# Performance work log

Hardware: AMD Instinct MI355X
Metric: run time of the kernel (lower is better)

## Reference

```python
import jax, jax.numpy as jnp
import numpy as np

N = 50000
E = 800000
EPS = 1e-5
# per-layer (in_dim, heads, out_dim, concat) matching GraphEncoder defaults
LAYERS = [(16, 4, 32, True), (128, 4, 32, True), (128, 4, 32, True), (128, 1, 128, False)]


def setup_inputs() -> dict:
    key = jax.random.key(0)
    ks = jax.random.split(key, 32)
    rn = lambda k, shape: jax.random.normal(k, shape, jnp.float32) * 0.1
    inp = {}
    inp["node_types"] = jax.random.randint(ks[0], (N,), 0, 3)
    inp["edge_index"] = jax.random.randint(ks[1], (2, E), 0, N)
    inp["emb"] = rn(ks[2], (3, 16))
    i = 3
    for li, (ind, h, od, _) in enumerate(LAYERS):
        inp[f"Wl{li}"] = rn(ks[i], (ind, h * od)); i += 1
        inp[f"Wr{li}"] = rn(ks[i], (ind, h * od)); i += 1
        inp[f"att{li}"] = rn(ks[i], (h, od)); i += 1
        inp[f"b{li}"] = rn(ks[i], (h * od if li < 3 else od,)); i += 1
    inp["ln_g"] = jnp.ones((4, 128), jnp.float32)
    inp["ln_b"] = jnp.zeros((4, 128), jnp.float32)
    return inp


def gatv2_layer(x, src, dst, Wl, Wr, att, b, heads, out_dim, concat):
    # PyG GATv2Conv (share_weights=False, negative_slope=0.2, self-loops added by caller)
    n = x.shape[0]
    xl = (x @ Wl).reshape(n, heads, out_dim)  # source transform (messages)
    xr = (x @ Wr).reshape(n, heads, out_dim)  # target transform
    e = jax.nn.leaky_relu(xl[src] + xr[dst], 0.2)          # [E', H, D]
    logit = jnp.einsum('ehd,hd->eh', e, att)               # [E', H]
    lmax = jax.ops.segment_max(logit, dst, num_segments=n)  # segment softmax over dst
    p = jnp.exp(logit - lmax[dst])
    z = jax.ops.segment_sum(p, dst, num_segments=n)
    alpha = p / z[dst]                                      # every node has a self-loop -> z > 0
    out = jax.ops.segment_sum(xl[src] * alpha[..., None], dst, num_segments=n)  # [n, H, D]
    out = out.reshape(n, heads * out_dim) if concat else out.mean(axis=1)
    return out + b


def layer_norm(x, g, b):
    mu = x.mean(-1, keepdims=True)
    var = ((x - mu) ** 2).mean(-1, keepdims=True)
    return (x - mu) / jnp.sqrt(var + EPS) * g + b


def reference(node_types, edge_index, emb, Wl0, Wr0, att0, b0, Wl1, Wr1, att1, b1,
              Wl2, Wr2, att2, b2, Wl3, Wr3, att3, b3, ln_g, ln_b):
    n = node_types.shape[0]
    loops = jnp.arange(n)
    src = jnp.concatenate([edge_index[0], loops])
    dst = jnp.concatenate([edge_index[1], loops])
    x = emb[node_types]
    params = [(Wl0, Wr0, att0, b0), (Wl1, Wr1, att1, b1), (Wl2, Wr2, att2, b2), (Wl3, Wr3, att3, b3)]
    for li, ((Wl, Wr, att, b), (_, h, od, concat)) in enumerate(zip(params, LAYERS)):
        res = x
        x = gatv2_layer(x, src, dst, Wl, Wr, att, b, h, od, concat)
        if x.shape[-1] == res.shape[-1]:
            x = x + res
        x = jax.nn.relu(layer_norm(x, ln_g[li], ln_b[li]))
    return x
```

## Files before the change

### kernel.cpp

```cpp
#include <hip/hip_runtime.h>

__global__ void GraphEncoder_20555713479231_kernel() {}

using hfrag8 = __attribute__((ext_vector_type(8))) _Float16;
using facc4  = __attribute__((ext_vector_type(4))) float;
using h2     = __attribute__((ext_vector_type(2))) _Float16;

__device__ __forceinline__ unsigned short f2h_bits(float f) {
  union { _Float16 h; unsigned short u; } c;
  c.h = (_Float16)f;
  return c.u;
}
__device__ __forceinline__ unsigned packh(float a, float b) {
  return (unsigned)f2h_bits(a) | ((unsigned)f2h_bits(b) << 16);
}
__device__ __forceinline__ h2 u2h(unsigned u) {
  union { unsigned u; h2 h; } c;
  c.u = u;
  return c.h;
}
__device__ __forceinline__ unsigned h22u(h2 h) {
  union { h2 h; unsigned u; } c;
  c.h = h;
  return c.u;
}
__device__ __forceinline__ float h2f_lo(unsigned u) { return (float)u2h(u).x; }
__device__ __forceinline__ float h2f_hi(unsigned u) { return (float)u2h(u).y; }

__global__ __launch_bounds__(256) void k_hist(const int* __restrict__ dst,
                                              int* __restrict__ deg, int e) {
  int i = blockIdx.x * blockDim.x + threadIdx.x;
  if (i < e) atomicAdd(&deg[dst[i]], 1);
}

__global__ __launch_bounds__(256) void k_scan1(const int* __restrict__ deg,
                                               int* __restrict__ off,
                                               int* __restrict__ bsum, int n) {
  __shared__ int wsum[4];
  int tid = threadIdx.x;
  int gid = blockIdx.x * 256 + tid;
  int lane = tid & 63, wid = tid >> 6;
  int v = (gid < n) ? (deg[gid] + 1) : 0;
  int x = v;
  #pragma unroll
  for (int d = 1; d < 64; d <<= 1) {
    int t = __shfl_up(x, d);
    if (lane >= d) x += t;
  }
  if (lane == 63) wsum[wid] = x;
  __syncthreads();
  int wpre = 0;
  for (int k = 0; k < wid; ++k) wpre += wsum[k];
  if (gid < n) off[gid] = wpre + x - v;
  if (tid == 0) {
    int t = 0;
    #pragma unroll
    for (int k = 0; k < 4; ++k) t += wsum[k];
    bsum[blockIdx.x] = t;
  }
}

__global__ __launch_bounds__(256) void k_scan2(int* __restrict__ bsum,
                                               int* __restrict__ off, int nb, int n) {
  __shared__ int wsum[4];
  int tid = threadIdx.x;
  int lane = tid & 63, wid = tid >> 6;
  int v = (tid < nb) ? bsum[tid] : 0;
  int x = v;
  #pragma unroll
  for (int d = 1; d < 64; d <<= 1) {
    int t = __shfl_up(x, d);
    if (lane >= d) x += t;
  }
  if (lane == 63) wsum[wid] = x;
  __syncthreads();
  int wpre = 0;
  for (int k = 0; k < wid; ++k) wpre += wsum[k];
  if (tid < nb) bsum[tid] = wpre + x - v;
  if (tid == 0) {
    int t = 0;
    #pragma unroll
    for (int k = 0; k < 4; ++k) t += wsum[k];
    off[n] = t;
  }
}

__global__ __launch_bounds__(256) void k_scan3(int* __restrict__ off,
                                               const int* __restrict__ bsum,
                                               int* __restrict__ pos,
                                               int* __restrict__ csr, int n) {
  int gid = blockIdx.x * 256 + threadIdx.x;
  if (gid < n) {
    int o = off[gid] + bsum[blockIdx.x];
    off[gid] = o;
    csr[o] = gid;
    pos[gid] = o + 1;
  }
}

__global__ __launch_bounds__(256) void k_fill(const int* __restrict__ src,
                                              const int* __restrict__ dst,
                                              int* __restrict__ pos,
                                              int* __restrict__ csr, int e) {
  int i = blockIdx.x * blockDim.x + threadIdx.x;
  if (i < e) {
    int d = dst[i];
    int p = atomicAdd(&pos[d], 1);
    csr[p] = src[i];
  }
}

__global__ __launch_bounds__(256)
void k_pack3(const float* __restrict__ wl1, const float* __restrict__ wr1,
             const float* __restrict__ wl2, const float* __restrict__ wr2,
             const float* __restrict__ wl3, const float* __restrict__ wr3,
             const float* __restrict__ emb,
             const float* __restrict__ wl0, const float* __restrict__ wr0,
             unsigned short* __restrict__ bp,
             unsigned* __restrict__ tlb, float* __restrict__ trf) {
  int b = blockIdx.x;
  if (b < 384) {
    int idx = b * 256 + threadIdx.x;
    int layer = idx >> 15;
    int r = idx & 32767;
    int j = r & 7, lane = (r >> 3) & 63, ct = (r >> 9) & 15, t = r >> 13;
    int k = t * 32 + (lane >> 4) * 8 + j;
    int c = ct * 16 + (lane & 15);
    const float* wl = (layer == 0) ? wl1 : ((layer == 1) ? wl2 : wl3);
    const float* wr = (layer == 0) ? wr1 : ((layer == 1) ? wr2 : wr3);
    float v = (c < 128) ? wl[k * 128 + c] : wr[k * 128 + (c - 128)];
    bp[idx] = f2h_bits(v);
  } else {
    int tid = threadIdx.x;
    if (tid >= 192) return;
    int row = tid >> 6, cp = tid & 63, c0 = cp * 2;
    float al0 = 0.f, al1 = 0.f, ar0 = 0.f, ar1 = 0.f;
    #pragma unroll
    for (int k = 0; k < 16; ++k) {
      float ev = emb[row * 16 + k];
      al0 += ev * wl0[k * 128 + c0];
      al1 += ev * wl0[k * 128 + c0 + 1];
      ar0 += ev * wr0[k * 128 + c0];
      ar1 += ev * wr0[k * 128 + c0 + 1];
    }
    tlb[row * 64 + cp] = packh(al0, al1);
    *(float2*)(trf + row * 128 + c0) = make_float2(ar0, ar1);
  }
}

__global__ __launch_bounds__(256)
void k_agg0(const int* __restrict__ off, const int* __restrict__ csr,
            const int* __restrict__ types,
            const unsigned* __restrict__ tlb, const float* __restrict__ trf,
            const float* __restrict__ att, const float* __restrict__ bias,
            const float* __restrict__ lng, const float* __restrict__ lnb,
            unsigned* __restrict__ yout, int n) {
  int v = (blockIdx.x * blockDim.x + threadIdx.x) >> 6;
  int lane = threadIdx.x & 63;
  if (v >= n) return;
  v = __builtin_amdgcn_readfirstlane(v);
  int beg = off[v], end = off[v + 1];
  int c0 = 0, c1 = 0, c2 = 0;
  for (int base = beg; base < end; base += 64) {
    int e = base + lane;
    bool act = e < end;
    int u = act ? csr[e] : 0;
    int ty = act ? types[u] : 3;
    c0 += __popcll(__ballot(ty == 0));
    c1 += __popcll(__ballot(ty == 1));
    c2 += __popcll(__ballot(ty == 2));
  }
  float cnt[3] = {(float)c0, (float)c1, (float)c2};
  int f0 = lane * 2;
  int tyv = types[v];
  float2 xrv = *(const float2*)(trf + tyv * 128 + f0);
  float a0 = att[f0], a1 = att[f0 + 1];
  float s = 0.f, O0 = 0.f, O1 = 0.f;
  #pragma unroll
  for (int ty = 0; ty < 3; ++ty) {
    unsigned p = tlb[ty * 64 + lane];
    float x0 = h2f_lo(p), x1 = h2f_hi(p);
    float t0 = x0 + xrv.x; t0 = t0 > 0.f ? t0 : 0.2f * t0;
    float t1 = x1 + xrv.y; t1 = t1 > 0.f ? t1 : 0.2f * t1;
    float c = t0 * a0 + t1 * a1;
    c += __shfl_xor(c, 1);
    c += __shfl_xor(c, 2);
    c += __shfl_xor(c, 4);
    c += __shfl_xor(c, 8);
    float w = cnt[ty] * __expf(c);
    s += w;
    O0 = fmaf(w, x0, O0);
    O1 = fmaf(w, x1, O1);
  }
  float inv = 1.f / s;
  float o0 = O0 * inv + bias[f0];
  float o1 = O1 * inv + bias[f0 + 1];
  float sum = o0 + o1, sq = o0 * o0 + o1 * o1;
  #pragma unroll
  for (int d2 = 1; d2 < 64; d2 <<= 1) {
    sum += __shfl_xor(sum, d2);
    sq += __shfl_xor(sq, d2);
  }
  float mu = sum * (1.f / 128.f);
  float var = sq * (1.f / 128.f) - mu * mu;
  float rstd = rsqrtf(var + 1e-5f);
  float y0 = fmaxf((o0 - mu) * rstd * lng[f0] + lnb[f0], 0.f);
  float y1 = fmaxf((o1 - mu) * rstd * lng[f0 + 1] + lnb[f0 + 1], 0.f);
  yout[(size_t)v * 64 + lane] = packh(y0, y1);
}

__global__ __launch_bounds__(256)
void k_gemm(const unsigned* __restrict__ x, const unsigned short* __restrict__ bp,
            unsigned* __restrict__ xlo, unsigned* __restrict__ xro, int nstrips, int n) {
  int wave = (blockIdx.x * 256 + threadIdx.x) >> 6;
  int lane = threadIdx.x & 63;
  if (wave >= nstrips) return;
  int r0 = wave * 16;
  int row = r0 + (lane & 15);
  if (row >= n) row = n - 1;
  int quad = lane >> 4;
  const unsigned* ap = x + (size_t)row * 64;
  hfrag8 a[4];
  #pragma unroll
  for (int t = 0; t < 4; ++t) a[t] = *(const hfrag8*)(ap + t * 16 + quad * 4);
  unsigned short* xloS = (unsigned short*)xlo;
  unsigned short* xroS = (unsigned short*)xro;
  int rbase = r0 + quad * 4;
  #pragma unroll
  for (int ct = 0; ct < 16; ++ct) {
    facc4 acc = {0.f, 0.f, 0.f, 0.f};
    #pragma unroll
    for (int t = 0; t < 4; ++t) {
      hfrag8 b = *(const hfrag8*)(bp + (size_t)(((t * 16 + ct) * 64 + lane) * 8));
      acc = __builtin_amdgcn_mfma_f32_16x16x32_f16(a[t], b, acc, 0, 0, 0);
    }
    int col = (ct & 7) * 16 + (lane & 15);
    unsigned short* dstp = (ct < 8) ? xloS : xroS;
    #pragma unroll
    for (int i = 0; i < 4; ++i) {
      int r = rbase + i;
      if (r < n) dstp[(size_t)r * 128 + col] = f2h_bits(acc[i]);
    }
  }
}

__global__ __launch_bounds__(256)
void k_agg(const int* __restrict__ off, const int* __restrict__ csr,
           const unsigned* __restrict__ xl, const unsigned* __restrict__ xr,
           const float* __restrict__ att, const float* __restrict__ bias,
           const unsigned* __restrict__ xres,
           const float* __restrict__ lng, const float* __restrict__ lnb,
           unsigned* __restrict__ ybf, float* __restrict__ yf32, int n, int wide) {
  int v = (blockIdx.x * blockDim.x + threadIdx.x) >> 6;
  int lane = threadIdx.x & 63;
  if (v >= n) return;
  v = __builtin_amdgcn_readfirstlane(v);
  int f0 = lane * 2;
  h2 a2;
  a2.x = (_Float16)att[f0];
  a2.y = (_Float16)att[f0 + 1];
  h2 r2 = u2h(xr[(size_t)v * 64 + lane]);
  h2 k02 = {(_Float16)0.2f, (_Float16)0.2f};
  int beg = off[v], end = off[v + 1];
  int last = end - 1;
  const unsigned* xlp = xl + lane;
  int iA = csr[beg];
  int iB = csr[min(beg + 1, last)];
  int iC = csr[min(beg + 2, last)];
  int iD = csr[min(beg + 3, last)];
  unsigned pA = xlp[(size_t)iA * 64];
  unsigned pB = xlp[(size_t)iB * 64];
  unsigned pC = xlp[(size_t)iC * 64];
  unsigned pD = xlp[(size_t)iD * 64];
  float sa = 0.f, Oa0 = 0.f, Oa1 = 0.f;
  float sb = 0.f, Ob0 = 0.f, Ob1 = 0.f;
  for (int e = beg; e < end; e += 2) {
    int i4 = csr[min(e + 4, last)];
    int i5 = csr[min(e + 5, last)];
    unsigned p4 = xlp[(size_t)i4 * 64];
    unsigned p5 = xlp[(size_t)i5 * 64];
    h2 xa = u2h(pA), xb = u2h(pB);
    h2 ta = xa + r2;
    h2 tb = xb + r2;
    h2 la = __builtin_elementwise_max(ta, ta * k02);
    h2 lb = __builtin_elementwise_max(tb, tb * k02);
    h2 da = la * a2;
    h2 db = lb * a2;
    h2 cp;
    cp.x = da.x + da.y;
    cp.y = db.x + db.y;
    unsigned cu = h22u(cp);
    cu = h22u(u2h(cu) + u2h((unsigned)__shfl_xor((int)cu, 1)));
    cu = h22u(u2h(cu) + u2h((unsigned)__shfl_xor((int)cu, 2)));
    cu = h22u(u2h(cu) + u2h((unsigned)__shfl_xor((int)cu, 4)));
    cu = h22u(u2h(cu) + u2h((unsigned)__shfl_xor((int)cu, 8)));
    if (wide) {
      cu = h22u(u2h(cu) + u2h((unsigned)__shfl_xor((int)cu, 16)));
      cu = h22u(u2h(cu) + u2h((unsigned)__shfl_xor((int)cu, 32)));
    }
    h2 cf = u2h(cu);
    float wa = __expf((float)cf.x);
    float wb = (e + 1 < end) ? __expf((float)cf.y) : 0.f;
    sa += wa; Oa0 = fmaf(wa, (float)xa.x, Oa0); Oa1 = fmaf(wa, (float)xa.y, Oa1);
    sb += wb; Ob0 = fmaf(wb, (float)xb.x, Ob0); Ob1 = fmaf(wb, (float)xb.y, Ob1);
    pA = pC; pB = pD; pC = p4; pD = p5;
  }
  float s = sa + sb;
  float O0 = Oa0 + Ob0, O1 = Oa1 + Ob1;
  float inv = 1.f / s;
  float o0 = O0 * inv + bias[f0];
  float o1 = O1 * inv + bias[f0 + 1];
  if (xres) {
    unsigned rs = xres[(size_t)v * 64 + lane];
    o0 += h2f_lo(rs);
    o1 += h2f_hi(rs);
  }
  float sum = o0 + o1, sq = o0 * o0 + o1 * o1;
  #pragma unroll
  for (int d2 = 1; d2 < 64; d2 <<= 1) {
    sum += __shfl_xor(sum, d2);
    sq += __shfl_xor(sq, d2);
  }
  float mu = sum * (1.f / 128.f);
  float var = sq * (1.f / 128.f) - mu * mu;
  float rstd = rsqrtf(var + 1e-5f);
  float y0 = fmaxf((o0 - mu) * rstd * lng[f0] + lnb[f0], 0.f);
  float y1 = fmaxf((o1 - mu) * rstd * lng[f0 + 1] + lnb[f0 + 1], 0.f);
  if (yf32) {
    *(float2*)(yf32 + (size_t)v * 128 + f0) = make_float2(y0, y1);
  } else {
    ybf[(size_t)v * 64 + lane] = packh(y0, y1);
  }
}

extern "C" void kernel_launch(void* const* d_in, const int* in_sizes, int n_in,
                              void* d_out, int out_size, void* d_ws, size_t ws_size,
                              hipStream_t stream) {
  (void)n_in; (void)out_size; (void)ws_size;
  const int* node_types = (const int*)d_in[0];
  const int* edge_index = (const int*)d_in[1];
  const float* emb = (const float*)d_in[2];
  const float* Wl0 = (const float*)d_in[3];
  const float* Wr0 = (const float*)d_in[4];
  const float* att0 = (const float*)d_in[5];
  const float* b0 = (const float*)d_in[6];
  const float* Wl1 = (const float*)d_in[7];
  const float* Wr1 = (const float*)d_in[8];
  const float* att1 = (const float*)d_in[9];
  const float* b1 = (const float*)d_in[10];
  const float* Wl2 = (const float*)d_in[11];
  const float* Wr2 = (const float*)d_in[12];
  const float* att2 = (const float*)d_in[13];
  const float* b2 = (const float*)d_in[14];
  const float* Wl3 = (const float*)d_in[15];
  const float* Wr3 = (const float*)d_in[16];
  const float* att3 = (const float*)d_in[17];
  const float* b3 = (const float*)d_in[18];
  const float* lng = (const float*)d_in[19];
  const float* lnb = (const float*)d_in[20];

  int n = in_sizes[0];
  int e = in_sizes[1] / 2;
  const int* srcp = edge_index;
  const int* dstp = edge_index + e;
  int nblocks = (n + 255) / 256;

  char* wsp = (char*)d_ws;
  size_t ofs = 0;
  int* deg = (int*)(wsp + ofs); ofs += (((size_t)n * 4) + 255) & ~(size_t)255;
  int* off = (int*)(wsp + ofs); ofs += (((size_t)(n + 1) * 4) + 255) & ~(size_t)255;
  int* csr = (int*)(wsp + ofs); ofs += (((size_t)(e + n) * 4) + 255) & ~(size_t)255;
  int* bsum = (int*)(wsp + ofs); ofs += (((size_t)nblocks * 4) + 255) & ~(size_t)255;
  unsigned* xlb = (unsigned*)(wsp + ofs); ofs += (((size_t)n * 64 * 4) + 255) & ~(size_t)255;
  unsigned* xrb = (unsigned*)(wsp + ofs); ofs += (((size_t)n * 64 * 4) + 255) & ~(size_t)255;
  unsigned* xcur = (unsigned*)(wsp + ofs); ofs += (((size_t)n * 64 * 4) + 255) & ~(size_t)255;
  unsigned short* bp = (unsigned short*)(wsp + ofs); ofs += 3 * 65536;
  unsigned* tlb = (unsigned*)(wsp + ofs); ofs += 1024;
  float* trf = (float*)(wsp + ofs); ofs += 2048;
  int* pos = deg;

  (void)hipMemsetAsync(deg, 0, (size_t)n * 4, stream);
  k_hist<<<(e + 255) / 256, 256, 0, stream>>>(dstp, deg, e);
  k_pack3<<<385, 256, 0, stream>>>(Wl1, Wr1, Wl2, Wr2, Wl3, Wr3,
                                   emb, Wl0, Wr0, bp, tlb, trf);
  k_scan1<<<nblocks, 256, 0, stream>>>(deg, off, bsum, n);
  k_scan2<<<1, 256, 0, stream>>>(bsum, off, nblocks, n);
  k_scan3<<<nblocks, 256, 0, stream>>>(off, bsum, pos, csr, n);
  k_fill<<<(e + 255) / 256, 256, 0, stream>>>(srcp, dstp, pos, csr, e);

  int aggBlocks = (n * 64 + 255) / 256;

  k_agg0<<<aggBlocks, 256, 0, stream>>>(off, csr, node_types, tlb, trf,
                                        att0, b0, lng, lnb, xcur, n);

  int nstrips = (n + 15) / 16;
  int gemmBlocks = (nstrips + 3) / 4;

  k_gemm<<<gemmBlocks, 256, 0, stream>>>(xcur, bp, xlb, xrb, nstrips, n);
  k_agg<<<aggBlocks, 256, 0, stream>>>(off, csr, xlb, xrb, att1, b1, xcur,
                                       lng + 128, lnb + 128, xcur, (float*)0, n, 0);
  k_gemm<<<gemmBlocks, 256, 0, stream>>>(xcur, bp + 32768, xlb, xrb, nstrips, n);
  k_agg<<<aggBlocks, 256, 0, stream>>>(off, csr, xlb, xrb, att2, b2, xcur,
                                       lng + 256, lnb + 256, xcur, (float*)0, n, 0);
  k_gemm<<<gemmBlocks, 256, 0, stream>>>(xcur, bp + 65536, xlb, xrb, nstrips, n);
  k_agg<<<aggBlocks, 256, 0, stream>>>(off, csr, xlb, xrb, att3, b3, xcur,
                                       lng + 384, lnb + 384, (unsigned*)0, (float*)d_out, n, 1);
}
```

Measured before the change: 414.0 us.

## Pack node types into 2-bit words and accumulate aggregation in packed fp16

Node types are packed into 2-bit fields, 16 per 32-bit word, inside the existing pack kernel. Layer-0 aggregation then gathers from a 12.5 KB table instead of the 200 KB int array, which cuts random-gather traffic. Separately, the per-edge weighted feature accumulation in the main aggregation kernel now uses packed half2 multiply-adds instead of four fp32 FMAs. The fp16 accumulation risks precision loss on high-degree nodes with large unnormalized weights.

```diff
diff --git a/kernel.cpp b/kernel.cpp
--- a/kernel.cpp
+++ b/kernel.cpp
@@ -116,8 +116,10 @@
              const float* __restrict__ wl3, const float* __restrict__ wr3,
              const float* __restrict__ emb,
              const float* __restrict__ wl0, const float* __restrict__ wr0,
+             const int* __restrict__ types, int n,
              unsigned short* __restrict__ bp,
-             unsigned* __restrict__ tlb, float* __restrict__ trf) {
+             unsigned* __restrict__ tlb, float* __restrict__ trf,
+             unsigned* __restrict__ ptypes) {
   int b = blockIdx.x;
   if (b < 384) {
     int idx = b * 256 + threadIdx.x;
@@ -130,7 +132,7 @@
     const float* wr = (layer == 0) ? wr1 : ((layer == 1) ? wr2 : wr3);
     float v = (c < 128) ? wl[k * 128 + c] : wr[k * 128 + (c - 128)];
     bp[idx] = f2h_bits(v);
-  } else {
+  } else if (b == 384) {
     int tid = threadIdx.x;
     if (tid >= 192) return;
     int row = tid >> 6, cp = tid & 63, c0 = cp * 2;
@@ -145,12 +147,25 @@
     }
     tlb[row * 64 + cp] = packh(al0, al1);
     *(float2*)(trf + row * 128 + c0) = make_float2(ar0, ar1);
+  } else {
+    int i = (b - 385) * 256 + threadIdx.x;
+    int npk = (n + 15) >> 4;
+    if (i < npk) {
+      unsigned pw = 0;
+      #pragma unroll
+      for (int j = 0; j < 16; ++j) {
+        int u = i * 16 + j;
+        int ty = (u < n) ? (types[u] & 3) : 3;
+        pw |= ((unsigned)ty) << (2 * j);
+      }
+      ptypes[i] = pw;
+    }
   }
 }
 
 __global__ __launch_bounds__(256)
 void k_agg0(const int* __restrict__ off, const int* __restrict__ csr,
-            const int* __restrict__ types,
+            const unsigned* __restrict__ ptypes,
             const unsigned* __restrict__ tlb, const float* __restrict__ trf,
             const float* __restrict__ att, const float* __restrict__ bias,
             const float* __restrict__ lng, const float* __restrict__ lnb,
@@ -165,14 +180,16 @@
     int e = base + lane;
     bool act = e < end;
     int u = act ? csr[e] : 0;
-    int ty = act ? types[u] : 3;
+    unsigned pw = ptypes[u >> 4];
+    int ty = act ? (int)((pw >> ((u & 15) * 2)) & 3) : 3;
     c0 += __popcll(__ballot(ty == 0));
     c1 += __popcll(__ballot(ty == 1));
     c2 += __popcll(__ballot(ty == 2));
   }
   float cnt[3] = {(float)c0, (float)c1, (float)c2};
   int f0 = lane * 2;
-  int tyv = types[v];
+  unsigned pwv = ptypes[v >> 4];
+  int tyv = (int)((pwv >> ((v & 15) * 2)) & 3);
   float2 xrv = *(const float2*)(trf + tyv * 128 + f0);
   float a0 = att[f0], a1 = att[f0 + 1];
   float s = 0.f, O0 = 0.f, O1 = 0.f;
@@ -272,8 +289,9 @@
   unsigned pB = xlp[(size_t)iB * 64];
   unsigned pC = xlp[(size_t)iC * 64];
   unsigned pD = xlp[(size_t)iD * 64];
-  float sa = 0.f, Oa0 = 0.f, Oa1 = 0.f;
-  float sb = 0.f, Ob0 = 0.f, Ob1 = 0.f;
+  float sa = 0.f, sb = 0.f;
+  h2 Oa = {(_Float16)0.f, (_Float16)0.f};
+  h2 Ob = {(_Float16)0.f, (_Float16)0.f};
   for (int e = beg; e < end; e += 2) {
     int i4 = csr[min(e + 4, last)];
     int i5 = csr[min(e + 5, last)];
@@ -301,12 +319,19 @@
     h2 cf = u2h(cu);
     float wa = __expf((float)cf.x);
     float wb = (e + 1 < end) ? __expf((float)cf.y) : 0.f;
-    sa += wa; Oa0 = fmaf(wa, (float)xa.x, Oa0); Oa1 = fmaf(wa, (float)xa.y, Oa1);
-    sb += wb; Ob0 = fmaf(wb, (float)xb.x, Ob0); Ob1 = fmaf(wb, (float)xb.y, Ob1);
+    sa += wa;
+    sb += wb;
+    _Float16 wah = (_Float16)wa;
+    _Float16 wbh = (_Float16)wb;
+    h2 wa2 = {wah, wah};
+    h2 wb2 = {wbh, wbh};
+    Oa = wa2 * xa + Oa;
+    Ob = wb2 * xb + Ob;
     pA = pC; pB = pD; pC = p4; pD = p5;
   }
   float s = sa + sb;
-  float O0 = Oa0 + Ob0, O1 = Oa1 + Ob1;
+  float O0 = (float)Oa.x + (float)Ob.x;
+  float O1 = (float)Oa.y + (float)Ob.y;
   float inv = 1.f / s;
   float o0 = O0 * inv + bias[f0];
   float o1 = O1 * inv + bias[f0 + 1];
@@ -377,12 +402,16 @@
   unsigned short* bp = (unsigned short*)(wsp + ofs); ofs += 3 * 65536;
   unsigned* tlb = (unsigned*)(wsp + ofs); ofs += 1024;
   float* trf = (float*)(wsp + ofs); ofs += 2048;
+  unsigned* ptypes = (unsigned*)(wsp + ofs); ofs += ((((size_t)(n + 15) / 16) * 4) + 255) & ~(size_t)255;
   int* pos = deg;
 
   (void)hipMemsetAsync(deg, 0, (size_t)n * 4, stream);
   k_hist<<<(e + 255) / 256, 256, 0, stream>>>(dstp, deg, e);
-  k_pack3<<<385, 256, 0, stream>>>(Wl1, Wr1, Wl2, Wr2, Wl3, Wr3,
-                                   emb, Wl0, Wr0, bp, tlb, trf);
+  int npk = (n + 15) / 16;
+  int packGrid = 385 + (npk + 255) / 256;
+  k_pack3<<<packGrid, 256, 0, stream>>>(Wl1, Wr1, Wl2, Wr2, Wl3, Wr3,
+                                        emb, Wl0, Wr0, node_types, n,
+                                        bp, tlb, trf, ptypes);
   k_scan1<<<nblocks, 256, 0, stream>>>(deg, off, bsum, n);
   k_scan2<<<1, 256, 0, stream>>>(bsum, off, nblocks, n);
   k_scan3<<<nblocks, 256, 0, stream>>>(off, bsum, pos, csr, n);
@@ -390,7 +419,7 @@
 
   int aggBlocks = (n * 64 + 255) / 256;
 
-  k_agg0<<<aggBlocks, 256, 0, stream>>>(off, csr, node_types, tlb, trf,
+  k_agg0<<<aggBlocks, 256, 0, stream>>>(off, csr, ptypes, tlb, trf,
                                         att0, b0, lng, lnb, xcur, n);
 
   int nstrips = (n + 15) / 16;
```

New measurement: 408.7 us. Within noise of the previous version (-1.3%).
